# Kernel tuning notes

Hardware: AMD Instinct MI355X
Metric: run time of the kernel (lower is better)

## Reference

```python
import jax, jax.numpy as jnp
import numpy as np


def setup_inputs() -> dict:
    key = jax.random.key(0)
    k1, k2 = jax.random.split(key)
    B, T = 8192, 1024
    confidences = jax.random.uniform(k1, (B, T), dtype=jnp.float32)
    accuracies = jax.random.bernoulli(k2, 0.5, (B, T)).astype(jnp.float32)
    return {"confidences": confidences, "accuracies": accuracies}


def reference(confidences, accuracies):
    # exclusive cumulative product of (1 - conf): prod_{s<t} (1 - conf[:, s])
    no_buzz = 1.0 - confidences                      # [B, T]
    cum = jnp.cumprod(no_buzz, axis=1)               # inclusive cumprod
    excl = jnp.concatenate([jnp.ones_like(cum[:, :1]), cum[:, :-1]], axis=1)
    buzz_probs = confidences * excl                  # [B, T]
    system_scores = jnp.sum(buzz_probs * accuracies, axis=1)   # [B]
    correction = 1.0 - jnp.sum(buzz_probs, axis=1)             # [B]
    system_scores = system_scores + correction * accuracies[:, -1]
    return -jnp.mean(system_scores)
```

## Files before the change

### kernel.cpp

```cpp
#include <hip/hip_runtime.h>


#define TLEN 1024
#define NSEG 4
#define SEGW 256
#define WAVES_PER_BLOCK 16

__global__ __launch_bounds__(1024)
void buzz_loss_partial(const float* __restrict__ conf,
                       const float* __restrict__ acc,
                       float* __restrict__ partial) {
    const int lane = threadIdx.x & 63;
    const int wave = threadIdx.x >> 6;
    const long long row = (long long)blockIdx.x * WAVES_PER_BLOCK + wave;

    const float* crow = conf + row * TLEN;
    const float* arow = acc  + row * TLEN;

    float4 cv[NSEG], av[NSEG];
    #pragma unroll
    for (int s = 0; s < NSEG; ++s) {
        cv[s] = ((const float4*)(crow + s * SEGW))[lane];
        av[s] = ((const float4*)(arow + s * SEGW))[lane];
    }

    float carry = 1.0f;
    float sba = 0.0f, sb = 0.0f;
    float alast = 0.0f;

    #pragma unroll
    for (int s = 0; s < NSEG; ++s) {
        float c[4] = {cv[s].x, cv[s].y, cv[s].z, cv[s].w};
        float a[4] = {av[s].x, av[s].y, av[s].z, av[s].w};

        float p = (1.0f - c[0]) * (1.0f - c[1]) * (1.0f - c[2]) * (1.0f - c[3]);

        float incl = p;
        #pragma unroll
        for (int off = 1; off < 64; off <<= 1) {
            float v = __shfl_up(incl, off, 64);
            if (lane >= off) incl *= v;
        }
        float prefix = __shfl_up(incl, 1, 64);
        if (lane == 0) prefix = 1.0f;
        float run = carry * prefix;

        #pragma unroll
        for (int k = 0; k < 4; ++k) {
            float b = c[k] * run;
            sba += b * a[k];
            sb  += b;
            run *= (1.0f - c[k]);
        }

        carry *= __shfl(incl, 63, 64);

        if (s == NSEG - 1) alast = __shfl(a[3], 63, 64);
    }

    #pragma unroll
    for (int off = 32; off; off >>= 1) {
        sba += __shfl_xor(sba, off, 64);
        sb  += __shfl_xor(sb,  off, 64);
    }
    float score = sba + (1.0f - sb) * alast;

    __shared__ float smem[WAVES_PER_BLOCK];
    if (lane == 0) smem[wave] = score;
    __syncthreads();
    if (threadIdx.x == 0) {
        float s = 0.0f;
        #pragma unroll
        for (int w = 0; w < WAVES_PER_BLOCK; ++w) s += smem[w];
        partial[blockIdx.x] = s;
    }
}

__global__ __launch_bounds__(512)
void buzz_loss_reduce(const float* __restrict__ partial, float* __restrict__ out,
                      float neg_inv_b, int n) {
    const int tid = threadIdx.x;
    float v = (tid < n) ? partial[tid] : 0.0f;
    #pragma unroll
    for (int off = 32; off; off >>= 1) v += __shfl_xor(v, off, 64);
    __shared__ float smem[8];
    if ((tid & 63) == 0) smem[tid >> 6] = v;
    __syncthreads();
    if (tid == 0) {
        float s = 0.0f;
        #pragma unroll
        for (int w = 0; w < 8; ++w) s += smem[w];
        out[0] = s * neg_inv_b;
    }
}

extern "C" void kernel_launch(void* const* d_in, const int* in_sizes, int n_in,
                              void* d_out, int out_size, void* d_ws, size_t ws_size,
                              hipStream_t stream) {
    const float* conf = (const float*)d_in[0];
    const float* acc  = (const float*)d_in[1];
    float* out = (float*)d_out;
    float* partial = (float*)d_ws;

    const int total = in_sizes[0];
    const int B = total / TLEN;
    const int blocks = B / WAVES_PER_BLOCK;

    buzz_loss_partial<<<blocks, 64 * WAVES_PER_BLOCK, 0, stream>>>(conf, acc, partial);
    buzz_loss_reduce<<<1, 512, 0, stream>>>(partial, out, -1.0f / (float)B, blocks);
}
```

Before: 90.38 us.

## Give each lane a contiguous 16-element chunk so one wave scan covers the row

Each lane now owns a contiguous 16-element slice of the row instead of four strided float4 segments. One 64-lane multiplicative scan then covers the whole row, replacing four scans, and the two sum reductions are folded into one via sba - alast*sb. This cuts shuffle and scan work per row. In exchange, each lane's float4 loads are strided by 64 bytes across the wave, which may make global-load coalescing worse, and the sequential per-lane product chain gets longer.

```diff
diff --git a/kernel.cpp b/kernel.cpp
--- a/kernel.cpp
+++ b/kernel.cpp
@@ -2,8 +2,7 @@
 
 
 #define TLEN 1024
-#define NSEG 4
-#define SEGW 256
+#define CHUNK 16
 #define WAVES_PER_BLOCK 16
 
 __global__ __launch_bounds__(1024)
@@ -14,56 +13,58 @@
     const int wave = threadIdx.x >> 6;
     const long long row = (long long)blockIdx.x * WAVES_PER_BLOCK + wave;
 
-    const float* crow = conf + row * TLEN;
-    const float* arow = acc  + row * TLEN;
+    const float* cbase = conf + row * TLEN + lane * CHUNK;
+    const float* abase = acc  + row * TLEN + lane * CHUNK;
 
-    float4 cv[NSEG], av[NSEG];
+    float4 cv[4], av[4];
     #pragma unroll
-    for (int s = 0; s < NSEG; ++s) {
-        cv[s] = ((const float4*)(crow + s * SEGW))[lane];
-        av[s] = ((const float4*)(arow + s * SEGW))[lane];
+    for (int k = 0; k < 4; ++k) {
+        cv[k] = ((const float4*)cbase)[k];
+        av[k] = ((const float4*)abase)[k];
     }
 
-    float carry = 1.0f;
-    float sba = 0.0f, sb = 0.0f;
-    float alast = 0.0f;
-
+    float p = 1.0f;
     #pragma unroll
-    for (int s = 0; s < NSEG; ++s) {
-        float c[4] = {cv[s].x, cv[s].y, cv[s].z, cv[s].w};
-        float a[4] = {av[s].x, av[s].y, av[s].z, av[s].w};
-
-        float p = (1.0f - c[0]) * (1.0f - c[1]) * (1.0f - c[2]) * (1.0f - c[3]);
-
-        float incl = p;
-        #pragma unroll
-        for (int off = 1; off < 64; off <<= 1) {
-            float v = __shfl_up(incl, off, 64);
-            if (lane >= off) incl *= v;
-        }
-        float prefix = __shfl_up(incl, 1, 64);
-        if (lane == 0) prefix = 1.0f;
-        float run = carry * prefix;
-
-        #pragma unroll
-        for (int k = 0; k < 4; ++k) {
-            float b = c[k] * run;
-            sba += b * a[k];
-            sb  += b;
-            run *= (1.0f - c[k]);
-        }
-
-        carry *= __shfl(incl, 63, 64);
-
-        if (s == NSEG - 1) alast = __shfl(a[3], 63, 64);
+    for (int k = 0; k < 4; ++k) {
+        p *= (1.0f - cv[k].x);
+        p *= (1.0f - cv[k].y);
+        p *= (1.0f - cv[k].z);
+        p *= (1.0f - cv[k].w);
     }
 
+    float incl = p;
     #pragma unroll
-    for (int off = 32; off; off >>= 1) {
-        sba += __shfl_xor(sba, off, 64);
-        sb  += __shfl_xor(sb,  off, 64);
+    for (int off = 1; off < 64; off <<= 1) {
+        float v = __shfl_up(incl, off, 64);
+        if (lane >= off) incl *= v;
     }
-    float score = sba + (1.0f - sb) * alast;
+    float run = __shfl_up(incl, 1, 64);
+    if (lane == 0) run = 1.0f;
+
+    float sba = 0.0f, sb = 0.0f;
+#define STEP(CC, AA)                          \
+    {                                         \
+        float b = (CC) * run;                 \
+        sba = fmaf(b, (AA), sba);             \
+        sb += b;                              \
+        run *= (1.0f - (CC));                 \
+    }
+    #pragma unroll
+    for (int k = 0; k < 4; ++k) {
+        STEP(cv[k].x, av[k].x);
+        STEP(cv[k].y, av[k].y);
+        STEP(cv[k].z, av[k].z);
+        STEP(cv[k].w, av[k].w);
+    }
+#undef STEP
+
+    float alast = __shfl(av[3].w, 63, 64);
+
+    float v = fmaf(-alast, sb, sba);
+    #pragma unroll
+    for (int off = 32; off; off >>= 1)
+        v += __shfl_xor(v, off, 64);
+    float score = v + alast;
 
     __shared__ float smem[WAVES_PER_BLOCK];
     if (lane == 0) smem[wave] = score;
```

Result: no change. 91.88 us (+1.7%).
